# Kernel optimization log

Measured on AMD Instinct MI355X. Metric: run time of the kernel, lower is better.

The kernel has to match this reference:

```python
import jax, jax.numpy as jnp
import numpy as np

N = 100000
E = 1600000
IN_FEATS = 128
OUT_FEATS = 64


def setup_inputs() -> dict:
    key = jax.random.key(0)
    ks = jax.random.split(key, 8)
    node_feat = jax.random.normal(ks[0], (N, IN_FEATS), dtype=jnp.float32)
    edge_feat = jax.random.normal(ks[1], (E, 1), dtype=jnp.float32)
    # Linear params (PyTorch Linear: y = x @ W^T + b; we store W already transposed as [in, out])
    W_node = jax.random.normal(ks[2], (IN_FEATS, OUT_FEATS), dtype=jnp.float32) / np.sqrt(IN_FEATS)
    b_node = jax.random.normal(ks[3], (OUT_FEATS,), dtype=jnp.float32) * 0.01
    W_edge = jax.random.normal(ks[4], (1, OUT_FEATS), dtype=jnp.float32)
    b_edge = jax.random.normal(ks[5], (OUT_FEATS,), dtype=jnp.float32) * 0.01
    src = jax.random.randint(ks[6], (E,), 0, N, dtype=jnp.int32)
    dst = jax.random.randint(ks[7], (E,), 0, N, dtype=jnp.int32)
    return {"node_feat": node_feat, "edge_feat": edge_feat, "W_node": W_node,
            "b_node": b_node, "W_edge": W_edge, "b_edge": b_edge,
            "src": src, "dst": dst}


def reference(node_feat, edge_feat, W_node, b_node, W_edge, b_edge, src, dst):
    n_nodes = node_feat.shape[0]
    # node linear: h = node_fc(node_feat)  -> [N, out]
    h = node_feat @ W_node + b_node
    # edge linear: he = edge_fc(edge_feat) -> [E, out]
    he = edge_feat @ W_edge + b_edge
    # u_add_e: m = h[src] + he  (gather + add)  -> [E, out]
    m = h[src] + he
    # mean aggregate over destination nodes (segment mean; 0 for isolated nodes, as in DGL)
    msg_sum = jax.ops.segment_sum(m, dst, num_segments=n_nodes)  # [N, out]
    deg = jax.ops.segment_sum(jnp.ones((dst.shape[0],), dtype=m.dtype), dst, num_segments=n_nodes)  # [N]
    h_new = msg_sum / jnp.maximum(deg, 1.0)[:, None]
    return h_new
```

## Files before the change

kernel.cpp:

```cpp
#include <hip/hip_runtime.h>

#define IN_F 128
#define OUT_F 64
#define BSH 6
#define BNODES 64
#define NBMAX 1600
#define MSC 6144
#define CAPB 2048

typedef __attribute__((ext_vector_type(8))) short short8;
typedef __attribute__((ext_vector_type(4))) float f32x4;

static __device__ __forceinline__ unsigned short f2bf(float f) {
    unsigned u = __float_as_uint(f);
    u += 0x7FFF + ((u >> 16) & 1);
    return (unsigned short)(u >> 16);
}

__global__ void prep(const float* __restrict__ W, unsigned short* __restrict__ Wt,
                     int* __restrict__ gcur, int nb) {
    int i = blockIdx.x * 256 + threadIdx.x;
    if (i < OUT_F * IN_F) {
        int o = i >> 7, k = i & 127;
        Wt[i] = f2bf(W[k * OUT_F + o]);
    }
    if (i < nb) gcur[i] = i * CAPB;
}

__global__ __launch_bounds__(256) void node_linear_mfma(const float* __restrict__ nf,
                                                        const unsigned short* __restrict__ Wt,
                                                        const float* __restrict__ bn,
                                                        unsigned short* __restrict__ h16,
                                                        int n_nodes, int n_tiles) {
    const int lane = threadIdx.x & 63;
    const int wid  = threadIdx.x >> 6;
    const int l15  = lane & 15;
    const int kq   = lane >> 4;

    short8 bfrag[4][4];
#pragma unroll
    for (int c = 0; c < 4; ++c)
#pragma unroll
        for (int ks = 0; ks < 4; ++ks)
            bfrag[c][ks] = *(const short8*)&Wt[(c * 16 + l15) * IN_F + ks * 32 + kq * 8];

    float bv[4];
#pragma unroll
    for (int c = 0; c < 4; ++c) bv[c] = bn[c * 16 + l15];

    for (int tile = blockIdx.x * 4 + wid; tile < n_tiles; tile += gridDim.x * 4) {
        int arow = tile * 16 + l15;
        if (arow >= n_nodes) arow = n_nodes - 1;
        const float* rp = nf + (size_t)arow * IN_F + kq * 8;

        f32x4 acc[4];
#pragma unroll
        for (int c = 0; c < 4; ++c) acc[c] = (f32x4){bv[c], bv[c], bv[c], bv[c]};

#pragma unroll
        for (int ks = 0; ks < 4; ++ks) {
            float4 x0 = *(const float4*)(rp + ks * 32);
            float4 x1 = *(const float4*)(rp + ks * 32 + 4);
            short8 af;
            af[0] = (short)f2bf(x0.x); af[1] = (short)f2bf(x0.y);
            af[2] = (short)f2bf(x0.z); af[3] = (short)f2bf(x0.w);
            af[4] = (short)f2bf(x1.x); af[5] = (short)f2bf(x1.y);
            af[6] = (short)f2bf(x1.z); af[7] = (short)f2bf(x1.w);
#pragma unroll
            for (int c = 0; c < 4; ++c)
                acc[c] = __builtin_amdgcn_mfma_f32_16x16x32_bf16(af, bfrag[c][ks], acc[c], 0, 0, 0);
        }

#pragma unroll
        for (int j = 0; j < 4; ++j) {
            int node = tile * 16 + kq * 4 + j;
            if (node < n_nodes) {
#pragma unroll
                for (int c = 0; c < 4; ++c)
                    h16[(size_t)node * OUT_F + c * 16 + l15] = f2bf(acc[c][j]);
            }
        }
    }
}

__global__ __launch_bounds__(1024) void multisplit(const int* __restrict__ src,
                                                   const int* __restrict__ dst,
                                                   const float* __restrict__ ef,
                                                   int* __restrict__ gcur,
                                                   int2* __restrict__ es,
                                                   int n_edges, int nb) {
    __shared__ int2 stage[MSC];
    __shared__ unsigned short sbuck[MSC];
    __shared__ int lhist[NBMAX];
    __shared__ int lbase[NBMAX];
    __shared__ int lcur[NBMAX];
    __shared__ int gbase[NBMAX];
    __shared__ int part[1024];

    const int t = threadIdx.x;
    const int cb = blockIdx.x * MSC;
    const int valid = min(MSC, n_edges - cb);
    if (valid <= 0) return;

    for (int i = t; i < nb; i += 1024) lhist[i] = 0;

    int   dr[6]; int sr[6]; float fr[6];
#pragma unroll
    for (int k = 0; k < 6; ++k) {
        int i = t + (k << 10);
        if (i < valid) { dr[k] = dst[cb + i]; sr[k] = src[cb + i]; fr[k] = ef[cb + i]; }
        else           { dr[k] = -1; sr[k] = 0; fr[k] = 0.f; }
    }
    __syncthreads();

#pragma unroll
    for (int k = 0; k < 6; ++k)
        if (dr[k] >= 0) atomicAdd(&lhist[dr[k] >> BSH], 1);
    __syncthreads();

    {
        const int b0 = t << 1;
        int v0 = (b0 < nb) ? lhist[b0] : 0;
        int v1 = (b0 + 1 < nb) ? lhist[b0 + 1] : 0;
        int s = v0 + v1;
        part[t] = s;
        __syncthreads();
        for (int off = 1; off < 1024; off <<= 1) {
            int x = (t >= off) ? part[t - off] : 0;
            __syncthreads();
            part[t] += x;
            __syncthreads();
        }
        int excl = part[t] - s;
        if (b0 < nb)     { lbase[b0] = excl;          lcur[b0] = excl; }
        if (b0 + 1 < nb) { lbase[b0 + 1] = excl + v0; lcur[b0 + 1] = excl + v0; }
    }
    __syncthreads();

    for (int b = t; b < nb; b += 1024) {
        int c = lhist[b];
        gbase[b] = c ? atomicAdd(&gcur[b], c) : 0;
    }
    __syncthreads();

#pragma unroll
    for (int k = 0; k < 6; ++k) {
        if (dr[k] >= 0) {
            int b = dr[k] >> BSH;
            int p = atomicAdd(&lcur[b], 1);
            int dl = dr[k] & (BNODES - 1);
            stage[p] = make_int2((dl << 17) | sr[k], __float_as_int(fr[k]));
            sbuck[p] = (unsigned short)b;
        }
    }
    __syncthreads();

    for (int i = t; i < valid; i += 1024) {
        int b = sbuck[i];
        int pos = gbase[b] + (i - lbase[b]);
        if (pos < (b + 1) * CAPB) es[pos] = stage[i];
    }
}

__global__ __launch_bounds__(512, 6) void aggregate(const unsigned short* __restrict__ h16,
                                                    const int2* __restrict__ es,
                                                    const int* __restrict__ gcur,
                                                    const float* __restrict__ We,
                                                    const float* __restrict__ be,
                                                    float* __restrict__ out, int n_nodes) {
    __shared__ int2 stage[CAPB];
    __shared__ int lhist[BNODES];
    __shared__ int lbase[BNODES];
    __shared__ int lcur[BNODES];
    __shared__ int sc[BNODES];

    const int t = threadIdx.x;
    const int bkt = blockIdx.x;
    const int s0 = bkt * CAPB;
    int cnt = gcur[bkt] - s0;
    if (cnt > CAPB) cnt = CAPB;

    if (t < BNODES) lhist[t] = 0;
    __syncthreads();

    int2 er[4];
#pragma unroll
    for (int k = 0; k < 4; ++k) {
        int i = t + (k << 9);
        if (i < cnt) er[k] = es[s0 + i];
    }
#pragma unroll
    for (int k = 0; k < 4; ++k) {
        int i = t + (k << 9);
        if (i < cnt) atomicAdd(&lhist[((unsigned)er[k].x) >> 17], 1);
    }
    __syncthreads();

    if (t < BNODES) sc[t] = lhist[t];
    __syncthreads();
    for (int off = 1; off < BNODES; off <<= 1) {
        int v = (t < BNODES && t >= off) ? sc[t - off] : 0;
        __syncthreads();
        if (t < BNODES) sc[t] += v;
        __syncthreads();
    }
    if (t < BNODES) { int e0 = sc[t] - lhist[t]; lbase[t] = e0; lcur[t] = e0; }
    __syncthreads();

#pragma unroll
    for (int k = 0; k < 4; ++k) {
        int i = t + (k << 9);
        if (i < cnt) {
            int b = ((unsigned)er[k].x) >> 17;
            int p = atomicAdd(&lcur[b], 1);
            stage[p] = er[k];
        }
    }
    __syncthreads();

    const int wid  = t >> 6;
    const int lane = t & 63;
    const int q    = lane >> 4;
    const int o4e  = (lane & 15) << 2;
    const float4 we4 = *(const float4*)&We[o4e];
    const float4 be4 = *(const float4*)&be[o4e];

#pragma unroll
    for (int p = 0; p < 4; ++p) {
        const int dlA = (wid << 3) + (p << 1);
        const int dlB = dlA + 1;
        const int jA = lbase[dlA], dgA = lhist[dlA];
        const int jB = lbase[dlB], dgB = lhist[dlB];
        float4 aA = make_float4(0.f, 0.f, 0.f, 0.f);
        float4 aB = make_float4(0.f, 0.f, 0.f, 0.f);
        float sxA = 0.f, sxB = 0.f;
        const int jm = dgA > dgB ? dgA : dgB;
        for (int j = 0; j < jm; j += 4) {
            int2 eA = make_int2(0, 0), eB = make_int2(0, 0);
            if (j + q < dgA) eA = stage[jA + j + q];
            if (j + q < dgB) eB = stage[jB + j + q];
            uint2 hA = make_uint2(0u, 0u), hB = make_uint2(0u, 0u);
            if (j + q < dgA) hA = *(const uint2*)&h16[((size_t)(eA.x & 0x1FFFF) << 6) + o4e];
            if (j + q < dgB) hB = *(const uint2*)&h16[((size_t)(eB.x & 0x1FFFF) << 6) + o4e];
            aA.x += __uint_as_float(hA.x << 16);
            aA.y += __uint_as_float(hA.x & 0xFFFF0000u);
            aA.z += __uint_as_float(hA.y << 16);
            aA.w += __uint_as_float(hA.y & 0xFFFF0000u);
            sxA  += __int_as_float(eA.y);
            aB.x += __uint_as_float(hB.x << 16);
            aB.y += __uint_as_float(hB.x & 0xFFFF0000u);
            aB.z += __uint_as_float(hB.y << 16);
            aB.w += __uint_as_float(hB.y & 0xFFFF0000u);
            sxB  += __int_as_float(eB.y);
        }
#define RED_(v) { v += __shfl_xor(v, 16, 64); v += __shfl_xor(v, 32, 64); }
        RED_(aA.x) RED_(aA.y) RED_(aA.z) RED_(aA.w) RED_(sxA)
        RED_(aB.x) RED_(aB.y) RED_(aB.z) RED_(aB.w) RED_(sxB)
#undef RED_
        if (q == 0) {
            int nodeA = (bkt << BSH) + dlA;
            if (nodeA < n_nodes) {
                float4 r = make_float4(0.f, 0.f, 0.f, 0.f);
                if (dgA > 0) {
                    float dgf = (float)dgA, inv = 1.f / dgf;
                    r.x = (aA.x + we4.x * sxA + dgf * be4.x) * inv;
                    r.y = (aA.y + we4.y * sxA + dgf * be4.y) * inv;
                    r.z = (aA.z + we4.z * sxA + dgf * be4.z) * inv;
                    r.w = (aA.w + we4.w * sxA + dgf * be4.w) * inv;
                }
                *(float4*)&out[((size_t)nodeA << 6) + o4e] = r;
            }
            int nodeB = (bkt << BSH) + dlB;
            if (nodeB < n_nodes) {
                float4 r = make_float4(0.f, 0.f, 0.f, 0.f);
                if (dgB > 0) {
                    float dgf = (float)dgB, inv = 1.f / dgf;
                    r.x = (aB.x + we4.x * sxB + dgf * be4.x) * inv;
                    r.y = (aB.y + we4.y * sxB + dgf * be4.y) * inv;
                    r.z = (aB.z + we4.z * sxB + dgf * be4.z) * inv;
                    r.w = (aB.w + we4.w * sxB + dgf * be4.w) * inv;
                }
                *(float4*)&out[((size_t)nodeB << 6) + o4e] = r;
            }
        }
    }
}

extern "C" void kernel_launch(void* const* d_in, const int* in_sizes, int n_in,
                              void* d_out, int out_size, void* d_ws, size_t ws_size,
                              hipStream_t stream) {
    const float* nf  = (const float*)d_in[0];
    const float* ef  = (const float*)d_in[1];
    const float* Wn  = (const float*)d_in[2];
    const float* bn  = (const float*)d_in[3];
    const float* We  = (const float*)d_in[4];
    const float* be  = (const float*)d_in[5];
    const int*   src = (const int*)d_in[6];
    const int*   dst = (const int*)d_in[7];
    float* out = (float*)d_out;

    const int n_nodes = in_sizes[0] / IN_F;
    const int n_edges = in_sizes[6];
    const int nb = (n_nodes + BNODES - 1) >> BSH;
    const int n_tiles = (n_nodes + 15) / 16;

    char* w = (char*)d_ws;
    unsigned short* h16 = (unsigned short*)w; w += (size_t)n_nodes * OUT_F * sizeof(unsigned short);
    int2* es  = (int2*)w; w += (size_t)nb * CAPB * sizeof(int2);
    int* gcur = (int*)w;  w += (size_t)NBMAX * sizeof(int);
    unsigned short* Wt = (unsigned short*)w; w += (size_t)OUT_F * IN_F * sizeof(unsigned short);

    prep<<<32, 256, 0, stream>>>(Wn, Wt, gcur, nb);
    node_linear_mfma<<<782, 256, 0, stream>>>(nf, Wt, bn, h16, n_nodes, n_tiles);
    multisplit<<<(n_edges + MSC - 1) / MSC, 1024, 0, stream>>>(src, dst, ef, gcur, es, n_edges, nb);
    aggregate<<<nb, 512, 0, stream>>>(h16, es, gcur, We, be, out, n_nodes);
}
```

Baseline: 87.43 us.

## Fuse node linear and edge multisplit into one block-specialized kernel; speed up aggregate scan

Merges the MFMA node-linear kernel and the edge multisplit kernel into one launch. Every fourth block runs the GEMM and the rest bucket edges, so the two independent stages overlap and one launch is saved. In aggregate, the per-bucket histogram becomes per-wave sub-histograms that are then summed. The barrier-heavy shared-memory prefix scan becomes a single-wave shuffle scan, and the occupancy hint is raised. The grid sizing gives more GEMM-role blocks than NLB, so some tiles are computed twice (same values written). The large shared-memory footprint of the multisplit path also applies to the GEMM-role blocks.

```diff
diff --git a/kernel.cpp b/kernel.cpp
--- a/kernel.cpp
+++ b/kernel.cpp
@@ -7,6 +7,7 @@
 #define NBMAX 1600
 #define MSC 6144
 #define CAPB 2048
+#define NLB 90
 
 typedef __attribute__((ext_vector_type(8))) short short8;
 typedef __attribute__((ext_vector_type(4))) float f32x4;
@@ -27,68 +28,13 @@
     if (i < nb) gcur[i] = i * CAPB;
 }
 
-__global__ __launch_bounds__(256) void node_linear_mfma(const float* __restrict__ nf,
-                                                        const unsigned short* __restrict__ Wt,
-                                                        const float* __restrict__ bn,
-                                                        unsigned short* __restrict__ h16,
-                                                        int n_nodes, int n_tiles) {
-    const int lane = threadIdx.x & 63;
-    const int wid  = threadIdx.x >> 6;
-    const int l15  = lane & 15;
-    const int kq   = lane >> 4;
-
-    short8 bfrag[4][4];
-#pragma unroll
-    for (int c = 0; c < 4; ++c)
-#pragma unroll
-        for (int ks = 0; ks < 4; ++ks)
-            bfrag[c][ks] = *(const short8*)&Wt[(c * 16 + l15) * IN_F + ks * 32 + kq * 8];
-
-    float bv[4];
-#pragma unroll
-    for (int c = 0; c < 4; ++c) bv[c] = bn[c * 16 + l15];
-
-    for (int tile = blockIdx.x * 4 + wid; tile < n_tiles; tile += gridDim.x * 4) {
-        int arow = tile * 16 + l15;
-        if (arow >= n_nodes) arow = n_nodes - 1;
-        const float* rp = nf + (size_t)arow * IN_F + kq * 8;
-
-        f32x4 acc[4];
-#pragma unroll
-        for (int c = 0; c < 4; ++c) acc[c] = (f32x4){bv[c], bv[c], bv[c], bv[c]};
-
-#pragma unroll
-        for (int ks = 0; ks < 4; ++ks) {
-            float4 x0 = *(const float4*)(rp + ks * 32);
-            float4 x1 = *(const float4*)(rp + ks * 32 + 4);
-            short8 af;
-            af[0] = (short)f2bf(x0.x); af[1] = (short)f2bf(x0.y);
-            af[2] = (short)f2bf(x0.z); af[3] = (short)f2bf(x0.w);
-            af[4] = (short)f2bf(x1.x); af[5] = (short)f2bf(x1.y);
-            af[6] = (short)f2bf(x1.z); af[7] = (short)f2bf(x1.w);
-#pragma unroll
-            for (int c = 0; c < 4; ++c)
-                acc[c] = __builtin_amdgcn_mfma_f32_16x16x32_bf16(af, bfrag[c][ks], acc[c], 0, 0, 0);
-        }
-
-#pragma unroll
-        for (int j = 0; j < 4; ++j) {
-            int node = tile * 16 + kq * 4 + j;
-            if (node < n_nodes) {
-#pragma unroll
-                for (int c = 0; c < 4; ++c)
-                    h16[(size_t)node * OUT_F + c * 16 + l15] = f2bf(acc[c][j]);
-            }
-        }
-    }
-}
-
-__global__ __launch_bounds__(1024) void multisplit(const int* __restrict__ src,
-                                                   const int* __restrict__ dst,
-                                                   const float* __restrict__ ef,
-                                                   int* __restrict__ gcur,
-                                                   int2* __restrict__ es,
-                                                   int n_edges, int nb) {
+__global__ __launch_bounds__(1024, 8) void fused_nl_ms(
+        const float* __restrict__ nf, const unsigned short* __restrict__ Wt,
+        const float* __restrict__ bn, unsigned short* __restrict__ h16,
+        int n_nodes, int n_tiles,
+        const int* __restrict__ src, const int* __restrict__ dst,
+        const float* __restrict__ ef, int* __restrict__ gcur,
+        int2* __restrict__ es, int n_edges, int nb) {
     __shared__ int2 stage[MSC];
     __shared__ unsigned short sbuck[MSC];
     __shared__ int lhist[NBMAX];
@@ -97,8 +43,65 @@
     __shared__ int gbase[NBMAX];
     __shared__ int part[1024];
 
+    const int bid = blockIdx.x;
     const int t = threadIdx.x;
-    const int cb = blockIdx.x * MSC;
+
+    if ((bid & 3) == 0) {
+        const int nlid = bid >> 2;
+        const int lane = t & 63;
+        const int wid  = t >> 6;
+        const int l15  = lane & 15;
+        const int kq   = lane >> 4;
+
+        short8 bfrag[4][4];
+#pragma unroll
+        for (int c = 0; c < 4; ++c)
+#pragma unroll
+            for (int ks = 0; ks < 4; ++ks)
+                bfrag[c][ks] = *(const short8*)&Wt[(c * 16 + l15) * IN_F + ks * 32 + kq * 8];
+
+        float bv[4];
+#pragma unroll
+        for (int c = 0; c < 4; ++c) bv[c] = bn[c * 16 + l15];
+
+        for (int tile = nlid * 16 + wid; tile < n_tiles; tile += NLB * 16) {
+            int arow = tile * 16 + l15;
+            if (arow >= n_nodes) arow = n_nodes - 1;
+            const float* rp = nf + (size_t)arow * IN_F + kq * 8;
+
+            f32x4 acc[4];
+#pragma unroll
+            for (int c = 0; c < 4; ++c) acc[c] = (f32x4){bv[c], bv[c], bv[c], bv[c]};
+
+#pragma unroll
+            for (int ks = 0; ks < 4; ++ks) {
+                float4 x0 = *(const float4*)(rp + ks * 32);
+                float4 x1 = *(const float4*)(rp + ks * 32 + 4);
+                short8 af;
+                af[0] = (short)f2bf(x0.x); af[1] = (short)f2bf(x0.y);
+                af[2] = (short)f2bf(x0.z); af[3] = (short)f2bf(x0.w);
+                af[4] = (short)f2bf(x1.x); af[5] = (short)f2bf(x1.y);
+                af[6] = (short)f2bf(x1.z); af[7] = (short)f2bf(x1.w);
+#pragma unroll
+                for (int c = 0; c < 4; ++c)
+                    acc[c] = __builtin_amdgcn_mfma_f32_16x16x32_bf16(af, bfrag[c][ks], acc[c], 0, 0, 0);
+            }
+
+#pragma unroll
+            for (int j = 0; j < 4; ++j) {
+                int node = tile * 16 + kq * 4 + j;
+                if (node < n_nodes) {
+#pragma unroll
+                    for (int c = 0; c < 4; ++c)
+                        h16[(size_t)node * OUT_F + c * 16 + l15] = f2bf(acc[j < 0 ? 0 : c][j]);
+                }
+            }
+        }
+        return;
+    }
+
+    const int ms_id = bid - (bid >> 2) - 1;
+    const int cb = ms_id * MSC;
     const int valid = min(MSC, n_edges - cb);
     if (valid <= 0) return;
 
@@ -162,17 +165,17 @@
     }
 }
 
-__global__ __launch_bounds__(512, 6) void aggregate(const unsigned short* __restrict__ h16,
+__global__ __launch_bounds__(512, 8) void aggregate(const unsigned short* __restrict__ h16,
                                                     const int2* __restrict__ es,
                                                     const int* __restrict__ gcur,
                                                     const float* __restrict__ We,
                                                     const float* __restrict__ be,
                                                     float* __restrict__ out, int n_nodes) {
     __shared__ int2 stage[CAPB];
+    __shared__ int lhist8[8][BNODES];
     __shared__ int lhist[BNODES];
     __shared__ int lbase[BNODES];
     __shared__ int lcur[BNODES];
-    __shared__ int sc[BNODES];
 
     const int t = threadIdx.x;
     const int bkt = blockIdx.x;
@@ -180,9 +183,10 @@
     int cnt = gcur[bkt] - s0;
     if (cnt > CAPB) cnt = CAPB;
 
-    if (t < BNODES) lhist[t] = 0;
-    __syncthreads();
-
+    ((int*)lhist8)[t] = 0;
+    __syncthreads();
+
+    const int wv = t >> 6;
     int2 er[4];
 #pragma unroll
     for (int k = 0; k < 4; ++k) {
@@ -192,19 +196,24 @@
 #pragma unroll
     for (int k = 0; k < 4; ++k) {
         int i = t + (k << 9);
-        if (i < cnt) atomicAdd(&lhist[((unsigned)er[k].x) >> 17], 1);
-    }
-    __syncthreads();
-
-    if (t < BNODES) sc[t] = lhist[t];
-    __syncthreads();
-    for (int off = 1; off < BNODES; off <<= 1) {
-        int v = (t < BNODES && t >= off) ? sc[t - off] : 0;
-        __syncthreads();
-        if (t < BNODES) sc[t] += v;
-        __syncthreads();
-    }
-    if (t < BNODES) { int e0 = sc[t] - lhist[t]; lbase[t] = e0; lcur[t] = e0; }
+        if (i < cnt) atomicAdd(&lhist8[wv][((unsigned)er[k].x) >> 17], 1);
+    }
+    __syncthreads();
+
+    if (t < BNODES) {
+        int v = 0;
+#pragma unroll
+        for (int w = 0; w < 8; ++w) v += lhist8[w][t];
+        lhist[t] = v;
+        int s = v;
+#pragma unroll
+        for (int off = 1; off < 64; off <<= 1) {
+            int x = __shfl_up(s, off, 64);
+            if (t >= off) s += x;
+        }
+        lbase[t] = s - v;
+        lcur[t]  = s - v;
+    }
     __syncthreads();
 
 #pragma unroll
@@ -218,7 +227,6 @@
     }
     __syncthreads();
 
-    const int wid  = t >> 6;
     const int lane = t & 63;
     const int q    = lane >> 4;
     const int o4e  = (lane & 15) << 2;
@@ -227,7 +235,7 @@
 
 #pragma unroll
     for (int p = 0; p < 4; ++p) {
-        const int dlA = (wid << 3) + (p << 1);
+        const int dlA = (wv << 3) + (p << 1);
         const int dlB = dlA + 1;
         const int jA = lbase[dlA], dgA = lhist[dlA];
         const int jB = lbase[dlB], dgB = lhist[dlB];
@@ -310,8 +318,13 @@
     int* gcur = (int*)w;  w += (size_t)NBMAX * sizeof(int);
     unsigned short* Wt = (unsigned short*)w; w += (size_t)OUT_F * IN_F * sizeof(unsigned short);
 
+    const int n_ms = (n_edges + MSC - 1) / MSC;
+    int grid = NLB + n_ms;
+    grid = grid + (grid + 2) / 3 + 1;
+    while ((grid + 3) / 4 < NLB || grid - (grid + 3) / 4 < n_ms) ++grid;
+
     prep<<<32, 256, 0, stream>>>(Wn, Wt, gcur, nb);
-    node_linear_mfma<<<782, 256, 0, stream>>>(nf, Wt, bn, h16, n_nodes, n_tiles);
-    multisplit<<<(n_edges + MSC - 1) / MSC, 1024, 0, stream>>>(src, dst, ef, gcur, es, n_edges, nb);
+    fused_nl_ms<<<grid, 1024, 0, stream>>>(nf, Wt, bn, h16, n_nodes, n_tiles,
+                                           src, dst, ef, gcur, es, n_edges, nb);
     aggregate<<<nb, 512, 0, stream>>>(h16, es, gcur, We, be, out, n_nodes);
 }
```

Result: slower. 100.9 us (+15.4%).

## Double bucket width and replace barrier-based scans with wave shuffle scans

Applied to the files above, without the earlier changes.

Bucket size grows from 64 to 128 destination nodes (bucket count halves, per-bucket capacity doubles, multisplit chunk shrinks to 4096 edges). The multisplit block-wide prefix scan, which used a barrier on every step, becomes a two-level wavefront __shfl_up scan. The aggregate kernel builds per-wave histograms to reduce LDS atomic contention and scans with shuffles. This cuts barrier count and atomic contention, in exchange for more multisplit blocks, larger LDS staging per aggregate block, and a higher occupancy hint that may cause register spilling.

```diff
diff --git a/kernel.cpp b/kernel.cpp
--- a/kernel.cpp
+++ b/kernel.cpp
@@ -2,11 +2,11 @@
 
 #define IN_F 128
 #define OUT_F 64
-#define BSH 6
-#define BNODES 64
-#define NBMAX 1600
-#define MSC 6144
-#define CAPB 2048
+#define BSH 7
+#define BNODES 128
+#define NBMAX 800
+#define MSC 4096
+#define CAPB 4096
 
 typedef __attribute__((ext_vector_type(8))) short short8;
 typedef __attribute__((ext_vector_type(4))) float f32x4;
@@ -92,10 +92,9 @@
     __shared__ int2 stage[MSC];
     __shared__ unsigned short sbuck[MSC];
     __shared__ int lhist[NBMAX];
-    __shared__ int lbase[NBMAX];
     __shared__ int lcur[NBMAX];
     __shared__ int gbase[NBMAX];
-    __shared__ int part[1024];
+    __shared__ int wtot[16];
 
     const int t = threadIdx.x;
     const int cb = blockIdx.x * MSC;
@@ -104,9 +103,9 @@
 
     for (int i = t; i < nb; i += 1024) lhist[i] = 0;
 
-    int   dr[6]; int sr[6]; float fr[6];
-#pragma unroll
-    for (int k = 0; k < 6; ++k) {
+    int dr[4]; int sr[4]; float fr[4];
+#pragma unroll
+    for (int k = 0; k < 4; ++k) {
         int i = t + (k << 10);
         if (i < valid) { dr[k] = dst[cb + i]; sr[k] = src[cb + i]; fr[k] = ef[cb + i]; }
         else           { dr[k] = -1; sr[k] = 0; fr[k] = 0.f; }
@@ -114,37 +113,40 @@
     __syncthreads();
 
 #pragma unroll
-    for (int k = 0; k < 6; ++k)
+    for (int k = 0; k < 4; ++k)
         if (dr[k] >= 0) atomicAdd(&lhist[dr[k] >> BSH], 1);
     __syncthreads();
 
-    {
-        const int b0 = t << 1;
-        int v0 = (b0 < nb) ? lhist[b0] : 0;
-        int v1 = (b0 + 1 < nb) ? lhist[b0 + 1] : 0;
-        int s = v0 + v1;
-        part[t] = s;
-        __syncthreads();
-        for (int off = 1; off < 1024; off <<= 1) {
-            int x = (t >= off) ? part[t - off] : 0;
-            __syncthreads();
-            part[t] += x;
-            __syncthreads();
-        }
-        int excl = part[t] - s;
-        if (b0 < nb)     { lbase[b0] = excl;          lcur[b0] = excl; }
-        if (b0 + 1 < nb) { lbase[b0 + 1] = excl + v0; lcur[b0 + 1] = excl + v0; }
-    }
+    const int wv = t >> 6, lane = t & 63;
+    int v = (t < nb) ? lhist[t] : 0;
+    int sc = v;
+#pragma unroll
+    for (int off = 1; off < 64; off <<= 1) {
+        int x = __shfl_up(sc, off, 64);
+        if (lane >= off) sc += x;
+    }
+    if (lane == 63) wtot[wv] = sc;
+    __syncthreads();
+    if (t < 16) {
+        int w = wtot[t];
+        int s2 = w;
+#pragma unroll
+        for (int off = 1; off < 16; off <<= 1) {
+            int x = __shfl_up(s2, off, 64);
+            if (t >= off) s2 += x;
+        }
+        wtot[t] = s2 - w;
+    }
+    __syncthreads();
+    if (t < nb) lcur[t] = wtot[wv] + (sc - v);
     __syncthreads();
 
     for (int b = t; b < nb; b += 1024) {
         int c = lhist[b];
         gbase[b] = c ? atomicAdd(&gcur[b], c) : 0;
     }
-    __syncthreads();
-
-#pragma unroll
-    for (int k = 0; k < 6; ++k) {
+#pragma unroll
+    for (int k = 0; k < 4; ++k) {
         if (dr[k] >= 0) {
             int b = dr[k] >> BSH;
             int p = atomicAdd(&lcur[b], 1);
@@ -157,22 +159,22 @@
 
     for (int i = t; i < valid; i += 1024) {
         int b = sbuck[i];
-        int pos = gbase[b] + (i - lbase[b]);
+        int pos = gbase[b] + (i - (lcur[b] - lhist[b]));
         if (pos < (b + 1) * CAPB) es[pos] = stage[i];
     }
 }
 
-__global__ __launch_bounds__(512, 6) void aggregate(const unsigned short* __restrict__ h16,
+__global__ __launch_bounds__(512, 8) void aggregate(const unsigned short* __restrict__ h16,
                                                     const int2* __restrict__ es,
                                                     const int* __restrict__ gcur,
                                                     const float* __restrict__ We,
                                                     const float* __restrict__ be,
                                                     float* __restrict__ out, int n_nodes) {
     __shared__ int2 stage[CAPB];
+    __shared__ int lhist8[8][BNODES];
     __shared__ int lhist[BNODES];
     __shared__ int lbase[BNODES];
     __shared__ int lcur[BNODES];
-    __shared__ int sc[BNODES];
 
     const int t = threadIdx.x;
     const int bkt = blockIdx.x;
@@ -180,35 +182,43 @@
     int cnt = gcur[bkt] - s0;
     if (cnt > CAPB) cnt = CAPB;
 
-    if (t < BNODES) lhist[t] = 0;
-    __syncthreads();
-
-    int2 er[4];
-#pragma unroll
-    for (int k = 0; k < 4; ++k) {
+    ((int*)lhist8)[t] = 0;
+    ((int*)lhist8)[t + 512] = 0;
+    __syncthreads();
+
+    const int wv = t >> 6;
+    int2 er[8];
+#pragma unroll
+    for (int k = 0; k < 8; ++k) {
         int i = t + (k << 9);
         if (i < cnt) er[k] = es[s0 + i];
     }
 #pragma unroll
-    for (int k = 0; k < 4; ++k) {
+    for (int k = 0; k < 8; ++k) {
         int i = t + (k << 9);
-        if (i < cnt) atomicAdd(&lhist[((unsigned)er[k].x) >> 17], 1);
-    }
-    __syncthreads();
-
-    if (t < BNODES) sc[t] = lhist[t];
-    __syncthreads();
-    for (int off = 1; off < BNODES; off <<= 1) {
-        int v = (t < BNODES && t >= off) ? sc[t - off] : 0;
-        __syncthreads();
-        if (t < BNODES) sc[t] += v;
-        __syncthreads();
-    }
-    if (t < BNODES) { int e0 = sc[t] - lhist[t]; lbase[t] = e0; lcur[t] = e0; }
-    __syncthreads();
-
-#pragma unroll
-    for (int k = 0; k < 4; ++k) {
+        if (i < cnt) atomicAdd(&lhist8[wv][((unsigned)er[k].x) >> 17], 1);
+    }
+    __syncthreads();
+
+    if (t < 64) {
+        int a = 0, b = 0;
+#pragma unroll
+        for (int w = 0; w < 8; ++w) { a += lhist8[w][t << 1]; b += lhist8[w][(t << 1) + 1]; }
+        lhist[t << 1] = a; lhist[(t << 1) + 1] = b;
+        int s = a + b;
+#pragma unroll
+        for (int off = 1; off < 64; off <<= 1) {
+            int x = __shfl_up(s, off, 64);
+            if (t >= off) s += x;
+        }
+        int excl = s - (a + b);
+        lbase[t << 1] = excl;       lcur[t << 1] = excl;
+        lbase[(t << 1) + 1] = excl + a; lcur[(t << 1) + 1] = excl + a;
+    }
+    __syncthreads();
+
+#pragma unroll
+    for (int k = 0; k < 8; ++k) {
         int i = t + (k << 9);
         if (i < cnt) {
             int b = ((unsigned)er[k].x) >> 17;
@@ -218,7 +228,6 @@
     }
     __syncthreads();
 
-    const int wid  = t >> 6;
     const int lane = t & 63;
     const int q    = lane >> 4;
     const int o4e  = (lane & 15) << 2;
@@ -226,8 +235,8 @@
     const float4 be4 = *(const float4*)&be[o4e];
 
 #pragma unroll
-    for (int p = 0; p < 4; ++p) {
-        const int dlA = (wid << 3) + (p << 1);
+    for (int p = 0; p < 8; ++p) {
+        const int dlA = (wv << 4) + (p << 1);
         const int dlB = dlA + 1;
         const int jA = lbase[dlA], dgA = lhist[dlA];
         const int jB = lbase[dlB], dgB = lhist[dlB];
```

After: 82.42 us. 1.06x faster.
